# Kernel optimization log

Measured on AMD Instinct MI355X. Metric: run time of the kernel, lower is better.

## Reference

```python
import jax, jax.numpy as jnp
import numpy as np

ALPHA = 0.2  # LeakyReLU negative slope


def setup_inputs() -> dict:
    key = jax.random.key(0)
    k0, k1, k2, k3 = jax.random.split(key, 4)
    N, H, W, T, V = 16, 32, 32, 16, 64
    h = jax.random.normal(k0, (N, H, W, T, V), jnp.float32)
    conv_w = jax.random.normal(k1, (3, 3, T, T), jnp.float32) * 0.05  # HWIO
    conv_b = jnp.zeros((T,), jnp.float32)
    a = jax.random.normal(k2, (2 * H * W, 1), jnp.float32) * 0.03  # ~xavier scale
    B = jax.random.uniform(k3, (V, V), jnp.float32)
    return {"h": h, "conv_w": conv_w, "conv_b": conv_b, "a": a, "B": B}


def reference(h, conv_w, conv_b, a, B):
    N, H, W, T, V = h.shape
    hv = jnp.transpose(h, (0, 4, 1, 2, 3))  # (N,V,H,W,T)

    # ConvMapping: 3x3 SAME conv over spatial dims with T as channels
    x = hv.reshape(N * V, H, W, T)
    y = jax.lax.conv_general_dilated(
        x, conv_w, (1, 1), 'SAME',
        dimension_numbers=('NHWC', 'HWIO', 'NHWC')) + conv_b
    Wh = y.reshape(N, V, H, W, T)

    # Attention logits. Original builds concat([Wh_i, Wh_j], dim=W) with trailing
    # layout (H, 2W, T) then row-major views it as (T, 2*H*W). We reproduce that
    # exact reinterpretation, but exploit additivity over i/j so the O(V^2)
    # pair tensor is never materialized.
    HW2 = 2 * H * W
    zeros = jnp.zeros_like(Wh)
    Cl = jnp.concatenate([Wh, zeros], axis=3).reshape(N, V, T, HW2)
    Cr = jnp.concatenate([zeros, Wh], axis=3).reshape(N, V, T, HW2)
    av = a[:, 0]
    Ei = jnp.einsum('bvtk,k->bvt', Cl, av)
    Ej = jnp.einsum('bvtk,k->bvt', Cr, av)
    e = jax.nn.leaky_relu(Ei[:, :, None, :] + Ej[:, None, :, :], ALPHA)  # (N,V,V,T)
    att = jax.nn.softmax(e, axis=-1)  # softmax over time dim, as in original

    # Symmetric-normalized adjacency: D^-1/2 (B + I, min-max scaled) D^-1/2
    adj = B + jnp.eye(V, dtype=B.dtype)
    adj = (adj - adj.min()) / (adj.max() - adj.min())
    d12 = 1.0 / jnp.sqrt(jnp.sum(adj, axis=1))
    adj_norm = adj * d12[:, None] * d12[None, :]

    # Aggregation: h_prime[b,p,t,i] = sum_j Wh[b,j,p,t] * att[b,i,j,t]
    # (replaces the original V^2 python loop + diag_embed matmuls)
    Whf = Wh.reshape(N, V, H * W, T)
    hp = jnp.einsum('bjpt,bijt->bpti', Whf, att)  # (N,HW,T,V)
    out = jnp.einsum('bpti,iv->bptv', hp, adj_norm)
    return jax.nn.elu(out.reshape(N, H, W, T, V))
```

## Files before the change

### kernel.cpp

```cpp
#include <hip/hip_runtime.h>
#include <hip/hip_bf16.h>
#include <math.h>

#define ALPHA_ 0.2f
#define N_ 16
#define H_ 32
#define W_ 32
#define T_ 16
#define V_ 64
#define P_ (H_*W_)

typedef __bf16 bf16x8 __attribute__((ext_vector_type(8)));
typedef float  f32x4  __attribute__((ext_vector_type(4)));

static __device__ inline bf16x8 zero8() {
    bf16x8 z;
    #pragma unroll
    for (int i = 0; i < 8; ++i) z[i] = (__bf16)0.f;
    return z;
}

static __device__ inline unsigned short bf16bits(float f) {
    __hip_bfloat16 b = __float2bfloat16(f);
    return *reinterpret_cast<unsigned short*>(&b);
}

static __device__ inline __bf16 tobf(float f) {
    unsigned short u = bf16bits(f);
    return *reinterpret_cast<__bf16*>(&u);
}

__global__ __launch_bounds__(256) void tr2_k(const float* __restrict__ X,
                                             __hip_bfloat16* __restrict__ Xt) {
    int bid = blockIdx.x;
    int b   = bid / 136;
    int r   = bid % 136;
    int hp  = r >> 2;
    int wq  = r & 3;
    int tid = threadIdx.x;

    __hip_bfloat16* dst = Xt + (((size_t)(b*34 + hp)*W_ + wq*8) * V_) * T_;

    if (hp == 0 || hp == 33) {
        uint4 z = {0u,0u,0u,0u};
        uint4* d = (uint4*)dst;
        #pragma unroll
        for (int k = 0; k < 4; ++k) d[tid + 256*k] = z;
        return;
    }
    int h = hp - 1;

    __shared__ __align__(16) unsigned sx[4096];

    int vq  = tid & 15;
    int tp4 = (tid >> 4) & 3;
    int w4  = tid >> 6;
    const float* Xb = X + (((size_t)(b*H_ + h)*W_ + wq*8) * T_) * V_ + vq*4;

    f32x4 xr[2][2][2];
    #pragma unroll
    for (int iw = 0; iw < 2; ++iw) {
        int wl = iw*4 + w4;
        #pragma unroll
        for (int th = 0; th < 2; ++th) {
            #pragma unroll
            for (int tk = 0; tk < 2; ++tk) {
                int ti = (th*4 + tp4)*2 + tk;
                xr[iw][th][tk] = *(const f32x4*)(Xb + ((size_t)wl*T_ + ti)*V_);
            }
        }
    }
    #pragma unroll
    for (int iw = 0; iw < 2; ++iw) {
        int wl = iw*4 + w4;
        #pragma unroll
        for (int th = 0; th < 2; ++th) {
            int tp = th*4 + tp4;
            uint4 pk;
            unsigned* pw = (unsigned*)&pk;
            #pragma unroll
            for (int k2 = 0; k2 < 4; ++k2)
                pw[k2] = (unsigned)bf16bits(xr[iw][th][0][k2])
                       | ((unsigned)bf16bits(xr[iw][th][1][k2]) << 16);
            *(uint4*)&sx[(wl*8 + tp)*64 + (vq ^ tp4)*4] = pk;
        }
    }
    __syncthreads();

    #pragma unroll
    for (int k = 0; k < 4; ++k) {
        int c   = tid + 256*k;
        int wl  = c >> 7;
        int vv  = (c >> 1) & 63;
        int thf = c & 1;
        uint4 o;
        unsigned* ow = (unsigned*)&o;
        #pragma unroll
        for (int q = 0; q < 4; ++q)
            ow[q] = sx[(wl*8 + thf*4 + q)*64 + ((vv >> 2) ^ q)*4 + (vv & 3)];
        *(uint4*)(dst + ((size_t)wl*V_ + vv)*T_ + thf*8) = o;
    }
}

__global__ __launch_bounds__(256) void conv_k(const __hip_bfloat16* __restrict__ Xt,
                                              const float* __restrict__ CW,
                                              const float* __restrict__ CB,
                                              const float* __restrict__ av,
                                              __hip_bfloat16* __restrict__ Whb,
                                              float* __restrict__ Eihi,
                                              float* __restrict__ Eihj) {
    __shared__ float sEi[4][16], sEj[4][16];

    int orig = blockIdx.x;
    int bi   = (orig & 7) * 256 + (orig >> 3);
    int b    = bi >> 7;
    int rem  = bi & 127;
    int h    = rem >> 2;
    int vg   = rem & 3, vb = vg * 16;

    int tid = threadIdx.x, lane = tid & 63, wc = tid >> 6;
    int lm = lane & 15, kg = lane >> 4;

    bf16x8 Bf01[3], Bf2[3];
    #pragma unroll
    for (int dw = 0; dw < 3; ++dw) {
        #pragma unroll
        for (int i = 0; i < 8; ++i) {
            int ti = (kg & 1)*8 + i;
            int dh = kg >> 1;
            Bf01[dw][i] = tobf(CW[((dh*3+dw)*16+ti)*16 + lm]);
            Bf2 [dw][i] = (kg < 2) ? tobf(CW[((6+dw)*16+ti)*16 + lm]) : (__bf16)0.f;
        }
    }
    float cb = CB[lm];
    f32x4 acc[8];
    #pragma unroll
    for (int wi = 0; wi < 8; ++wi) acc[wi] = (f32x4){cb, cb, cb, cb};

    const __hip_bfloat16* base01 =
        Xt + ((size_t)((b*34 + h + (kg>>1))*W_)*V_ + vb + lm)*T_ + (kg&1)*8;
    const __hip_bfloat16* base2  =
        Xt + ((size_t)((b*34 + h + 2)*W_)*V_ + vb + lm)*T_ + (kg&1)*8;

    #pragma unroll
    for (int u = 0; u < 10; ++u) {
        int wxu = wc*8 + u - 1;
        bf16x8 f01 = zero8(), f2 = zero8();
        if ((unsigned)wxu < (unsigned)W_) {
            f01 = *(const bf16x8*)(base01 + (size_t)wxu*(V_*T_));
            f2  = *(const bf16x8*)(base2  + (size_t)wxu*(V_*T_));
        }
        #pragma unroll
        for (int dw = 0; dw < 3; ++dw) {
            int wi = u - dw;
            if (wi >= 0 && wi < 8) {
                acc[wi] = __builtin_amdgcn_mfma_f32_16x16x32_bf16(f01, Bf01[dw], acc[wi], 0, 0, 0);
                acc[wi] = __builtin_amdgcn_mfma_f32_16x16x32_bf16(f2,  Bf2 [dw], acc[wi], 0, 0, 0);
            }
        }
    }

    float si[4] = {0.f,0.f,0.f,0.f}, sj[4] = {0.f,0.f,0.f,0.f};
    {
        const float* avb = av + (h & 1)*1024 + wc*8*16 + lm;
        #pragma unroll
        for (int wi = 0; wi < 8; ++wi) {
            float ai = avb[wi*16];
            float aj = avb[wi*16 + 512];
            #pragma unroll
            for (int r = 0; r < 4; ++r) {
                si[r] += acc[wi][r] * ai;
                sj[r] += acc[wi][r] * aj;
            }
        }
        #pragma unroll
        for (int off = 1; off < 16; off <<= 1) {
            #pragma unroll
            for (int r = 0; r < 4; ++r) {
                si[r] += __shfl_xor(si[r], off);
                sj[r] += __shfl_xor(sj[r], off);
            }
        }
    }
    if (lm == 0) {
        #pragma unroll
        for (int r = 0; r < 4; ++r) {
            sEi[wc][kg*4 + r] = si[r];
            sEj[wc][kg*4 + r] = sj[r];
        }
    }

    #pragma unroll
    for (int wi = 0; wi < 8; ++wi) {
        int p = h*W_ + wc*8 + wi;
        unsigned short u0 = bf16bits(acc[wi][0]);
        unsigned short u1 = bf16bits(acc[wi][1]);
        unsigned short u2 = bf16bits(acc[wi][2]);
        unsigned short u3 = bf16bits(acc[wi][3]);
        uint2 pk;
        pk.x = (unsigned)u0 | ((unsigned)u1 << 16);
        pk.y = (unsigned)u2 | ((unsigned)u3 << 16);
        *(uint2*)(Whb + ((size_t)(b*T_ + lm)*P_ + p)*V_ + vb + kg*4) = pk;
    }

    __syncthreads();
    if (tid < 16) {
        float a = sEi[0][tid] + sEi[1][tid] + sEi[2][tid] + sEi[3][tid];
        float c = sEj[0][tid] + sEj[1][tid] + sEj[2][tid] + sEj[3][tid];
        Eihi[((size_t)b*H_ + h)*V_ + vb + tid] = a;
        Eihj[((size_t)b*H_ + h)*V_ + vb + tid] = c;
    }
}

__global__ __launch_bounds__(256) void att_m_k(const float* __restrict__ Eihi,
                                               const float* __restrict__ Eihj,
                                               const float* __restrict__ Bm,
                                               __hip_bfloat16* __restrict__ Mt) {
    int b = blockIdx.x >> 6;
    int j = blockIdx.x & 63;
    int tid = threadIdx.x;
    __shared__ float sadj[64][65];
    __shared__ float s_att[64][17];
    __shared__ float sd[64];

    if (tid < 64) {
        int i = tid;
        for (int r = 0; r < 64; ++r) sadj[r][i] = Bm[r*64 + i];
        float mn = 1e30f, mx = -1e30f;
        #pragma unroll
        for (int v = 0; v < 64; ++v) {
            float x = sadj[i][v] + (v == i ? 1.f : 0.f);
            mn = fminf(mn, x);
            mx = fmaxf(mx, x);
        }
        #pragma unroll
        for (int off = 32; off > 0; off >>= 1) {
            mn = fminf(mn, __shfl_xor(mn, off));
            mx = fmaxf(mx, __shfl_xor(mx, off));
        }
        float inv = 1.f / (mx - mn);
        float rs = 0.f;
        #pragma unroll
        for (int v = 0; v < 64; ++v) {
            float x = (sadj[i][v] + (v == i ? 1.f : 0.f) - mn) * inv;
            rs += x;
            sadj[i][v] = x;
        }
        float d = rsqrtf(rs);
        sd[i] = d;

        const float* ebi = Eihi + (size_t)b*H_*V_;
        const float* ebj = Eihj + (size_t)b*H_*V_;
        float ev[16];
        float mxe = -1e30f;
        #pragma unroll
        for (int t = 0; t < 16; ++t) {
            float x = ebi[(2*t)*V_ + i] + ebi[(2*t+1)*V_ + i]
                    + ebj[(2*t)*V_ + j] + ebj[(2*t+1)*V_ + j];
            x = (x >= 0.f) ? x : ALPHA_ * x;
            ev[t] = x;
            mxe = fmaxf(mxe, x);
        }
        float s = 0.f;
        #pragma unroll
        for (int t = 0; t < 16; ++t) {
            ev[t] = __expf(ev[t] - mxe);
            s += ev[t];
        }
        float invs = d / s;
        #pragma unroll
        for (int t = 0; t < 16; ++t) s_att[i][t] = ev[t] * invs;
    }
    __syncthreads();

    int v = tid & 63, tq = tid >> 6;
    float acc[4] = {0.f, 0.f, 0.f, 0.f};
    for (int i = 0; i < 64; ++i) {
        float an = sadj[i][v];
        #pragma unroll
        for (int u = 0; u < 4; ++u) acc[u] += s_att[i][tq*4 + u] * an;
    }
    float dv = sd[v];
    #pragma unroll
    for (int u = 0; u < 4; ++u) {
        int t = tq*4 + u;
        Mt[(((size_t)b*T_ + t)*V_ + v)*V_ + j] = __float2bfloat16(acc[u] * dv);
    }
}

__global__ __launch_bounds__(256) void out_k(const __hip_bfloat16* __restrict__ Whb,
                                             const __hip_bfloat16* __restrict__ Mt,
                                             float* __restrict__ out) {
    int bi = blockIdx.x;
    int pc = bi & 7;
    int t  = (bi >> 3) & 15;
    int b  = bi >> 7;

    int tid  = threadIdx.x;
    int lane = tid & 63;
    int wid  = tid >> 6;
    int lm   = lane & 15;
    int lk   = lane >> 4;

    const __hip_bfloat16* Ab = Whb + ((size_t)(b*T_ + t)*P_ + pc*128) * V_;
    const __hip_bfloat16* Bb = Mt  + (size_t)(b*T_ + t) * (V_*V_);

    f32x4 acc[2][4];
    #pragma unroll
    for (int pt = 0; pt < 2; ++pt)
        #pragma unroll
        for (int vt = 0; vt < 4; ++vt) acc[pt][vt] = (f32x4){0.f,0.f,0.f,0.f};

    #pragma unroll
    for (int kf = 0; kf < 2; ++kf) {
        int ko = kf*32 + lk*8;
        bf16x8 a0 = *(const bf16x8*)(Ab + ((size_t)((wid*2+0)*16 + lm))*V_ + ko);
        bf16x8 a1 = *(const bf16x8*)(Ab + ((size_t)((wid*2+1)*16 + lm))*V_ + ko);
        #pragma unroll
        for (int vt = 0; vt < 4; ++vt) {
            bf16x8 bf = *(const bf16x8*)(Bb + ((size_t)(vt*16 + lm))*V_ + ko);
            acc[0][vt] = __builtin_amdgcn_mfma_f32_16x16x32_bf16(a0, bf, acc[0][vt], 0, 0, 0);
            acc[1][vt] = __builtin_amdgcn_mfma_f32_16x16x32_bf16(a1, bf, acc[1][vt], 0, 0, 0);
        }
    }

    #pragma unroll
    for (int pt = 0; pt < 2; ++pt) {
        #pragma unroll
        for (int vt = 0; vt < 4; ++vt) {
            #pragma unroll
            for (int r = 0; r < 4; ++r) {
                int p  = pc*128 + (wid*2 + pt)*16 + lk*4 + r;
                int vv = vt*16 + lm;
                float x = acc[pt][vt][r];
                x = (x > 0.f) ? x : (__expf(x) - 1.f);
                out[((size_t)(b*P_ + p)*T_ + t)*V_ + vv] = x;
            }
        }
    }
}

extern "C" void kernel_launch(void* const* d_in, const int* in_sizes, int n_in,
                              void* d_out, int out_size, void* d_ws, size_t ws_size,
                              hipStream_t stream) {
    const float* X  = (const float*)d_in[0];
    const float* CW = (const float*)d_in[1];
    const float* CB = (const float*)d_in[2];
    const float* av = (const float*)d_in[3];
    const float* Bm = (const float*)d_in[4];
    float* outp = (float*)d_out;

    __hip_bfloat16* Whb = (__hip_bfloat16*)d_ws;
    __hip_bfloat16* Mt  = Whb + (size_t)N_*T_*P_*V_;
    float* Eihi = (float*)(Mt + (size_t)N_*T_*V_*V_);
    float* Eihj = Eihi + (size_t)N_*H_*V_;

    __hip_bfloat16* Xt = (__hip_bfloat16*)d_out;

    tr2_k  <<<N_*34*4, 256, 0, stream>>>(X, Xt);
    conv_k <<<2048,    256, 0, stream>>>(Xt, CW, CB, av, Whb, Eihi, Eihj);
    att_m_k<<<N_*V_,   256, 0, stream>>>(Eihi, Eihj, Bm, Mt);
    out_k  <<<N_*T_*8, 256, 0, stream>>>(Whb, Mt, outp);
}
```

Before: 85.85 us.

## Recompute convolution inside output kernel instead of storing Wh to global memory

New measurement: 88.99 us. +3.7%, slower.

```diff
diff --git a/kernel.cpp b/kernel.cpp
--- a/kernel.cpp
+++ b/kernel.cpp
@@ -33,22 +33,13 @@
 __global__ __launch_bounds__(256) void tr2_k(const float* __restrict__ X,
                                              __hip_bfloat16* __restrict__ Xt) {
     int bid = blockIdx.x;
-    int b   = bid / 136;
-    int r   = bid % 136;
-    int hp  = r >> 2;
+    int b   = bid >> 7;
+    int r   = bid & 127;
+    int h   = r >> 2;
     int wq  = r & 3;
     int tid = threadIdx.x;
 
-    __hip_bfloat16* dst = Xt + (((size_t)(b*34 + hp)*W_ + wq*8) * V_) * T_;
-
-    if (hp == 0 || hp == 33) {
-        uint4 z = {0u,0u,0u,0u};
-        uint4* d = (uint4*)dst;
-        #pragma unroll
-        for (int k = 0; k < 4; ++k) d[tid + 256*k] = z;
-        return;
-    }
-    int h = hp - 1;
+    __hip_bfloat16* dst = Xt + (((size_t)(b*H_ + h)*W_ + wq*8) * V_) * T_;
 
     __shared__ __align__(16) unsigned sx[4096];
 
@@ -102,13 +93,12 @@
     }
 }
 
-__global__ __launch_bounds__(256) void conv_k(const __hip_bfloat16* __restrict__ Xt,
-                                              const float* __restrict__ CW,
-                                              const float* __restrict__ CB,
-                                              const float* __restrict__ av,
-                                              __hip_bfloat16* __restrict__ Whb,
-                                              float* __restrict__ Eihi,
-                                              float* __restrict__ Eihj) {
+__global__ __launch_bounds__(256) void ei_k(const __hip_bfloat16* __restrict__ Xt,
+                                            const float* __restrict__ CW,
+                                            const float* __restrict__ CB,
+                                            const float* __restrict__ av,
+                                            float* __restrict__ Eihi,
+                                            float* __restrict__ Eihj) {
     __shared__ float sEi[4][16], sEj[4][16];
 
     int orig = blockIdx.x;
@@ -137,18 +127,22 @@
     #pragma unroll
     for (int wi = 0; wi < 8; ++wi) acc[wi] = (f32x4){cb, cb, cb, cb};
 
-    const __hip_bfloat16* base01 =
-        Xt + ((size_t)((b*34 + h + (kg>>1))*W_)*V_ + vb + lm)*T_ + (kg&1)*8;
-    const __hip_bfloat16* base2  =
-        Xt + ((size_t)((b*34 + h + 2)*W_)*V_ + vb + lm)*T_ + (kg&1)*8;
+    int row01 = h - 1 + (kg >> 1);
+    bool r01ok = (unsigned)row01 < (unsigned)H_;
+    int row2 = h + 1;
+    bool r2ok = row2 < H_;
+    const __hip_bfloat16* b01 =
+        Xt + ((size_t)((b*H_ + (r01ok ? row01 : 0))*W_)*V_ + vb + lm)*T_ + (kg&1)*8;
+    const __hip_bfloat16* b2  =
+        Xt + ((size_t)((b*H_ + (r2ok ? row2 : 0))*W_)*V_ + vb + lm)*T_ + (kg&1)*8;
 
     #pragma unroll
     for (int u = 0; u < 10; ++u) {
         int wxu = wc*8 + u - 1;
         bf16x8 f01 = zero8(), f2 = zero8();
         if ((unsigned)wxu < (unsigned)W_) {
-            f01 = *(const bf16x8*)(base01 + (size_t)wxu*(V_*T_));
-            f2  = *(const bf16x8*)(base2  + (size_t)wxu*(V_*T_));
+            if (r01ok) f01 = *(const bf16x8*)(b01 + (size_t)wxu*(V_*T_));
+            if (r2ok)  f2  = *(const bf16x8*)(b2  + (size_t)wxu*(V_*T_));
         }
         #pragma unroll
         for (int dw = 0; dw < 3; ++dw) {
@@ -189,20 +183,6 @@
             sEj[wc][kg*4 + r] = sj[r];
         }
     }
-
-    #pragma unroll
-    for (int wi = 0; wi < 8; ++wi) {
-        int p = h*W_ + wc*8 + wi;
-        unsigned short u0 = bf16bits(acc[wi][0]);
-        unsigned short u1 = bf16bits(acc[wi][1]);
-        unsigned short u2 = bf16bits(acc[wi][2]);
-        unsigned short u3 = bf16bits(acc[wi][3]);
-        uint2 pk;
-        pk.x = (unsigned)u0 | ((unsigned)u1 << 16);
-        pk.y = (unsigned)u2 | ((unsigned)u3 << 16);
-        *(uint2*)(Whb + ((size_t)(b*T_ + lm)*P_ + p)*V_ + vb + kg*4) = pk;
-    }
-
     __syncthreads();
     if (tid < 16) {
         float a = sEi[0][tid] + sEi[1][tid] + sEi[2][tid] + sEi[3][tid];
@@ -288,55 +268,100 @@
     }
 }
 
-__global__ __launch_bounds__(256) void out_k(const __hip_bfloat16* __restrict__ Whb,
-                                             const __hip_bfloat16* __restrict__ Mt,
-                                             float* __restrict__ out) {
-    int bi = blockIdx.x;
-    int pc = bi & 7;
-    int t  = (bi >> 3) & 15;
-    int b  = bi >> 7;
-
-    int tid  = threadIdx.x;
-    int lane = tid & 63;
-    int wid  = tid >> 6;
-    int lm   = lane & 15;
-    int lk   = lane >> 4;
-
-    const __hip_bfloat16* Ab = Whb + ((size_t)(b*T_ + t)*P_ + pc*128) * V_;
-    const __hip_bfloat16* Bb = Mt  + (size_t)(b*T_ + t) * (V_*V_);
-
-    f32x4 acc[2][4];
-    #pragma unroll
-    for (int pt = 0; pt < 2; ++pt)
-        #pragma unroll
-        for (int vt = 0; vt < 4; ++vt) acc[pt][vt] = (f32x4){0.f,0.f,0.f,0.f};
-
-    #pragma unroll
-    for (int kf = 0; kf < 2; ++kf) {
-        int ko = kf*32 + lk*8;
-        bf16x8 a0 = *(const bf16x8*)(Ab + ((size_t)((wid*2+0)*16 + lm))*V_ + ko);
-        bf16x8 a1 = *(const bf16x8*)(Ab + ((size_t)((wid*2+1)*16 + lm))*V_ + ko);
-        #pragma unroll
-        for (int vt = 0; vt < 4; ++vt) {
-            bf16x8 bf = *(const bf16x8*)(Bb + ((size_t)(vt*16 + lm))*V_ + ko);
-            acc[0][vt] = __builtin_amdgcn_mfma_f32_16x16x32_bf16(a0, bf, acc[0][vt], 0, 0, 0);
-            acc[1][vt] = __builtin_amdgcn_mfma_f32_16x16x32_bf16(a1, bf, acc[1][vt], 0, 0, 0);
-        }
-    }
-
-    #pragma unroll
-    for (int pt = 0; pt < 2; ++pt) {
-        #pragma unroll
-        for (int vt = 0; vt < 4; ++vt) {
-            #pragma unroll
-            for (int r = 0; r < 4; ++r) {
-                int p  = pc*128 + (wid*2 + pt)*16 + lk*4 + r;
-                int vv = vt*16 + lm;
-                float x = acc[pt][vt][r];
-                x = (x > 0.f) ? x : (__expf(x) - 1.f);
-                out[((size_t)(b*P_ + p)*T_ + t)*V_ + vv] = x;
-            }
-        }
+__global__ __launch_bounds__(512, 2) void out2_k(const __hip_bfloat16* __restrict__ Xt,
+                                                 const float* __restrict__ CW,
+                                                 const float* __restrict__ CB,
+                                                 const __hip_bfloat16* __restrict__ Mt,
+                                                 float* __restrict__ out) {
+    __shared__ __align__(16) char sA[16*4624];
+
+    int orig = blockIdx.x;
+    int bi   = (orig & 7) * 64 + (orig >> 3);
+    int b    = bi >> 5;
+    int h    = bi & 31;
+
+    int tid = threadIdx.x, lane = tid & 63, wv = tid >> 6;
+    int lm = lane & 15, kg = lane >> 4;
+    int wc = wv & 3, vh = wv >> 2;
+
+    bf16x8 Bf01[3], Bf2[3];
+    #pragma unroll
+    for (int dw = 0; dw < 3; ++dw) {
+        #pragma unroll
+        for (int i = 0; i < 8; ++i) {
+            int ti = (kg & 1)*8 + i;
+            int dh = kg >> 1;
+            Bf01[dw][i] = tobf(CW[((dh*3+dw)*16+ti)*16 + lm]);
+            Bf2 [dw][i] = (kg < 2) ? tobf(CW[((6+dw)*16+ti)*16 + lm]) : (__bf16)0.f;
+        }
+    }
+    float cb = CB[lm];
+
+    int row01 = h - 1 + (kg >> 1);
+    bool r01ok = (unsigned)row01 < (unsigned)H_;
+    int row2 = h + 1;
+    bool r2ok = row2 < H_;
+    const __hip_bfloat16* b01 =
+        Xt + ((size_t)((b*H_ + (r01ok ? row01 : 0))*W_)*V_ + lm)*T_ + (kg&1)*8;
+    const __hip_bfloat16* b2  =
+        Xt + ((size_t)((b*H_ + (r2ok ? row2 : 0))*W_)*V_ + lm)*T_ + (kg&1)*8;
+
+    #pragma unroll 1
+    for (int s = 0; s < 2; ++s) {
+        int vb = (vh*2 + s) * 16;
+        f32x4 acc[8];
+        #pragma unroll
+        for (int wi = 0; wi < 8; ++wi) acc[wi] = (f32x4){cb, cb, cb, cb};
+
+        #pragma unroll
+        for (int u = 0; u < 10; ++u) {
+            int wxu = wc*8 + u - 1;
+            bf16x8 f01 = zero8(), f2 = zero8();
+            if ((unsigned)wxu < (unsigned)W_) {
+                size_t off = ((size_t)wxu*V_ + vb)*T_;
+                if (r01ok) f01 = *(const bf16x8*)(b01 + off);
+                if (r2ok)  f2  = *(const bf16x8*)(b2  + off);
+            }
+            #pragma unroll
+            for (int dw = 0; dw < 3; ++dw) {
+                int wi = u - dw;
+                if (wi >= 0 && wi < 8) {
+                    acc[wi] = __builtin_amdgcn_mfma_f32_16x16x32_bf16(f01, Bf01[dw], acc[wi], 0, 0, 0);
+                    acc[wi] = __builtin_amdgcn_mfma_f32_16x16x32_bf16(f2,  Bf2 [dw], acc[wi], 0, 0, 0);
+                }
+            }
+        }
+        #pragma unroll
+        for (int wi = 0; wi < 8; ++wi) {
+            int w = wc*8 + wi;
+            uint2 pk;
+            pk.x = (unsigned)bf16bits(acc[wi][0]) | ((unsigned)bf16bits(acc[wi][1]) << 16);
+            pk.y = (unsigned)bf16bits(acc[wi][2]) | ((unsigned)bf16bits(acc[wi][3]) << 16);
+            *(uint2*)(sA + lm*4624 + w*144 + (vb + kg*4)*2) = pk;
+        }
+    }
+    __syncthreads();
+
+    int vt = wv & 3, wt = wv >> 2;
+    #pragma unroll 1
+    for (int t = 0; t < 16; ++t) {
+        const __hip_bfloat16* mrow = Mt + ((size_t)(b*T_ + t)*V_ + vt*16 + lm)*V_ + kg*8;
+        const char* srow = sA + t*4624 + (wt*16 + lm)*144 + kg*16;
+        f32x4 o = (f32x4){0.f, 0.f, 0.f, 0.f};
+        #pragma unroll
+        for (int kf = 0; kf < 2; ++kf) {
+            bf16x8 a  = *(const bf16x8*)(mrow + kf*32);
+            bf16x8 bb = *(const bf16x8*)(srow + kf*64);
+            o = __builtin_amdgcn_mfma_f32_16x16x32_bf16(a, bb, o, 0, 0, 0);
+        }
+        f32x4 e;
+        #pragma unroll
+        for (int r = 0; r < 4; ++r) {
+            float x = o[r];
+            e[r] = (x > 0.f) ? x : (__expf(x) - 1.f);
+        }
+        float* op = out + (((size_t)(b*P_ + h*W_ + wt*16 + lm)*T_ + t)*V_ + vt*16 + kg*4);
+        *(f32x4*)op = e;
     }
 }
 
@@ -350,15 +375,13 @@
     const float* Bm = (const float*)d_in[4];
     float* outp = (float*)d_out;
 
-    __hip_bfloat16* Whb = (__hip_bfloat16*)d_ws;
-    __hip_bfloat16* Mt  = Whb + (size_t)N_*T_*P_*V_;
+    __hip_bfloat16* Xt = (__hip_bfloat16*)d_ws;
+    __hip_bfloat16* Mt = Xt + (size_t)N_*H_*W_*V_*T_;
     float* Eihi = (float*)(Mt + (size_t)N_*T_*V_*V_);
     float* Eihj = Eihi + (size_t)N_*H_*V_;
 
-    __hip_bfloat16* Xt = (__hip_bfloat16*)d_out;
-
-    tr2_k  <<<N_*34*4, 256, 0, stream>>>(X, Xt);
-    conv_k <<<2048,    256, 0, stream>>>(Xt, CW, CB, av, Whb, Eihi, Eihj);
+    tr2_k  <<<N_*H_*4, 256, 0, stream>>>(X, Xt);
+    ei_k   <<<2048,    256, 0, stream>>>(Xt, CW, CB, av, Eihi, Eihj);
     att_m_k<<<N_*V_,   256, 0, stream>>>(Eihi, Eihj, Bm, Mt);
-    out_k  <<<N_*T_*8, 256, 0, stream>>>(Whb, Mt, outp);
-}
+    out2_k <<<512,     512, 0, stream>>>(Xt, CW, CB, Mt, outp);
+}
```
